# Kernel optimization log

Hardware: AMD Instinct MI355X
Metric: run time of the kernel (lower is better)

## Reference

```python
import jax, jax.numpy as jnp
import numpy as np

BS, S, D, H = 4, 1024, 768, 12
NE, M, P = 42, 8, 500
IN_C, OUT_C = 3, 256
EMB, BLK, NL = 768, 64, 97


def setup_inputs() -> dict:
    key = jax.random.key(0)
    ks = jax.random.split(key, 16)
    seq_out = jax.random.normal(ks[0], (BS, S, D), jnp.float32)
    attention = jax.random.uniform(ks[1], (BS, H, S, S), jnp.float32)
    ent_tok = jax.random.randint(ks[2], (BS, NE, M), 0, 1022)
    ent_mask = (jax.random.uniform(ks[3], (BS, NE, M)) < 0.7).astype(jnp.float32)
    ent_mask = ent_mask.at[:, :, 0].set(1.0)  # every entity has >=1 mention
    hts = jax.random.randint(ks[4], (BS, P, 2), 0, NE)
    sc = 0.02
    return {
        'seq_out': seq_out,
        'attention': attention,
        'ent_tok': ent_tok,
        'ent_mask': ent_mask,
        'hts': hts,
        'W_liner': jax.random.normal(ks[5], (D, IN_C)) * sc,
        'b_liner': jnp.zeros((IN_C,), jnp.float32),
        'W_seg': jax.random.normal(ks[6], (IN_C, OUT_C)) * sc,
        'b_seg': jnp.zeros((OUT_C,), jnp.float32),
        'W_head': jax.random.normal(ks[7], (D + OUT_C, EMB)) * sc,
        'b_head': jnp.zeros((EMB,), jnp.float32),
        'W_tail': jax.random.normal(ks[8], (D + OUT_C, EMB)) * sc,
        'b_tail': jnp.zeros((EMB,), jnp.float32),
        'W_bil': jax.random.normal(ks[9], (EMB * BLK, NL)) * sc,
        'b_bil': jnp.zeros((NL,), jnp.float32),
    }


def reference(seq_out, attention, ent_tok, ent_mask, hts,
              W_liner, b_liner, W_seg, b_seg,
              W_head, b_head, W_tail, b_tail, W_bil, b_bil):
    bs, S_, d = seq_out.shape
    heads = attention.shape[1]
    # --- get_hrt: per-entity ragged pooling (offset=1 on token starts) ---
    idx = jnp.clip(ent_tok + 1, 0, S_ - 1)                   # [bs,ne,M]
    valid = ent_mask * (ent_tok + 1 < S_).astype(ent_mask.dtype)
    b_ix = jnp.arange(bs)[:, None, None]
    tok_emb = seq_out[b_ix, idx]                             # [bs,ne,M,d]
    neg = jnp.where(valid[..., None] > 0, tok_emb, jnp.float32(-1e30))
    e_emb = jax.nn.logsumexp(neg, axis=2)                    # [bs,ne,d]
    cnt = valid.sum(2)                                       # [bs,ne]
    e_emb = jnp.where((cnt > 0)[..., None], e_emb, 0.0)
    att_g = attention[b_ix, :, idx]                          # [bs,ne,M,H,S]
    e_att = (att_g * valid[..., None, None]).sum(2) / jnp.maximum(cnt, 1.0)[..., None, None]  # [bs,ne,H,S]
    e_att = jnp.where((cnt > 0)[..., None, None], e_att, 0.0)
    # --- get_channel_map: attention-weighted context contraction ---
    ht_att = jnp.einsum('bihs,bjhs->bijs', e_att, e_att) / heads  # [bs,ne,ne,S]
    ht_att = ht_att / (ht_att.sum(-1, keepdims=True) + 1e-5)
    feat = jnp.einsum('bijs,bsd->bijd', ht_att, seq_out)          # [bs,ne,ne,d]
    # --- liner + segmentation stand-in (pointwise) ---
    attn_map = (feat @ W_liner + b_liner) @ W_seg + b_seg         # [bs,ne,ne,OUT_C]
    # --- gather pair features ---
    bp = jnp.arange(bs)[:, None]
    h_i, t_i = hts[..., 0], hts[..., 1]
    h_t = attn_map[bp, h_i, t_i].reshape(-1, attn_map.shape[-1])  # [bs*P,OUT_C]
    hs = e_emb[bp, h_i].reshape(-1, d)
    ts = e_emb[bp, t_i].reshape(-1, d)
    hs = jnp.tanh(jnp.concatenate([hs, h_t], axis=1) @ W_head + b_head)
    ts = jnp.tanh(jnp.concatenate([ts, h_t], axis=1) @ W_tail + b_tail)
    # --- block bilinear classifier ---
    n = hs.shape[0]
    b1 = hs.reshape(n, EMB // BLK, BLK)
    b2 = ts.reshape(n, EMB // BLK, BLK)
    bl = (b1[:, :, :, None] * b2[:, :, None, :]).reshape(n, EMB * BLK)
    logits = bl @ W_bil + b_bil                                   # [bs*P, NL]
    return logits
```

## Files before the change

### kernel.cpp

```cpp
#include <hip/hip_runtime.h>
#include <hip/hip_bf16.h>
#include <math.h>

#define BSZ 4
#define SEQ 1024
#define DIM 768
#define NH 12
#define NEnt 42
#define MM 8
#define PPairs 500
#define INC 3
#define OUTC 256
#define EMB 768
#define BLKsz 64
#define NL 97
#define NPAIR (BSZ*PPairs)
#define XROWS 2048
#define NCHUNK 24

typedef __bf16 bf16x8 __attribute__((ext_vector_type(8)));
typedef __bf16 bf16x4 __attribute__((ext_vector_type(4)));
typedef float f32x4 __attribute__((ext_vector_type(4)));

#define OFF_EEMB  4096
#define OFF_EATT  520192
#define OFF_SP    4648960
#define OFF_XB    4698112
#define OFF_WHT   13086720
#define OFF_WT    16232448
#define OFF_HSB   25767936
#define OFF_TSB   28839936
#define OFF_PART  31911936

#define B_EEMB0 0
#define B_EATT0 168
#define B_SP0   2184
#define B_WHT0  3208
#define B_WT0   3592
#define B_ZERO0 4360
#define B_TOTAL 4362

__device__ __forceinline__ float ldin(const void* p, long long i, int f32) {
  if (f32) return ((const float*)p)[i];
  unsigned int u = (unsigned int)(((const unsigned short*)p)[i]) << 16;
  union { unsigned int u; float f; } c; c.u = u;
  return c.f;
}

__device__ __forceinline__ f32x4 ldin4(const void* p, long long i, int f32) {
  f32x4 r;
  if (f32) {
    r = *(const f32x4*)((const float*)p + i);
  } else {
    unsigned long long v = *(const unsigned long long*)((const unsigned short*)p + i);
    union { unsigned int u; float f; } c;
    c.u = (unsigned int)(v & 0xFFFFu) << 16;         r[0] = c.f;
    c.u = (unsigned int)((v >> 16) & 0xFFFFu) << 16; r[1] = c.f;
    c.u = (unsigned int)((v >> 32) & 0xFFFFu) << 16; r[2] = c.f;
    c.u = (unsigned int)((v >> 48) & 0xFFFFu) << 16; r[3] = c.f;
  }
  return r;
}

__device__ __forceinline__ float tanhf_fast(float x) {
  float ax = fabsf(x);
  float t = __expf(-2.0f*ax);
  float r = (1.0f - t)/(1.0f + t);
  return x < 0.0f ? -r : r;
}

__global__ void k_detect(const void* w_head, int* flag) {
  int tid = threadIdx.x;
  unsigned int word = ((const unsigned int*)w_head)[tid];
  union { unsigned int u; float f; } c;
  c.u = (word & 0xFFFFu) << 16;
  float v = fabsf(c.f);
  unsigned long long m = __ballot(v > 1.0f);
  if (tid == 0) flag[0] = (__popcll(m) >= 8) ? 1 : 0;
}

__global__ __launch_bounds__(256)
void k_stage1(const void* seq, const void* att, const int* etok,
              const void* emask, const void* wliner,
              const void* whead, const void* wtail, const void* wbil,
              const int* flag,
              float* e_emb, __bf16* e_att, float* sp,
              __bf16* whT, __bf16* wT, __bf16* Xb) {
  __shared__ float smem[64*98];
  int blk = blockIdx.x;
  int tid = threadIdx.x;
  int f32 = *flag;

  if (blk < B_EATT0) {
    int be = blk, b = be / NEnt;
    int* sidx = (int*)smem;
    float* sval = smem + 16;
    if (tid < MM) {
      int t = etok[be*MM + tid];
      int ip = t + 1;
      float v = ldin(emask, be*MM + tid, f32);
      sval[tid] = (ip < SEQ) ? v : 0.0f;
      sidx[tid] = ip < 0 ? 0 : (ip > SEQ-1 ? SEQ-1 : ip);
    }
    __syncthreads();
    float cnt = 0.0f;
#pragma unroll
    for (int m = 0; m < MM; m++) cnt += sval[m];
    for (int d = tid; d < DIM; d += 256) {
      float x[MM];
#pragma unroll
      for (int m = 0; m < MM; m++)
        x[m] = ldin(seq, ((long long)(b*SEQ) + sidx[m])*DIM + d, f32);
      float mx = -1e30f;
#pragma unroll
      for (int m = 0; m < MM; m++) if (sval[m] > 0.0f && x[m] > mx) mx = x[m];
      float s = 0.0f;
#pragma unroll
      for (int m = 0; m < MM; m++) if (sval[m] > 0.0f) s += expf(x[m] - mx);
      e_emb[(long long)be*DIM + d] = (cnt > 0.0f) ? (mx + logf(s)) : 0.0f;
    }
  } else if (blk < B_SP0) {
    int t1 = blk - B_EATT0;
    int h = t1 % NH, be = t1 / NH, b = be / NEnt;
    int* sidx = (int*)smem;
    float* sval = smem + 16;
    if (tid < MM) {
      int t = etok[be*MM + tid];
      int ip = t + 1;
      float v = ldin(emask, be*MM + tid, f32);
      sval[tid] = (ip < SEQ) ? v : 0.0f;
      sidx[tid] = ip < 0 ? 0 : (ip > SEQ-1 ? SEQ-1 : ip);
    }
    __syncthreads();
    float cnt = 0.0f;
#pragma unroll
    for (int m = 0; m < MM; m++) cnt += sval[m];
    float rs = (cnt > 0.0f) ? 1.0f/fmaxf(cnt, 1.0f) : 0.0f;
    long long abase = ((long long)(b*NH + h))*SEQ*SEQ;
    int s0 = tid*4;
    f32x4 acc = (f32x4){0,0,0,0};
#pragma unroll
    for (int m = 0; m < MM; m++)
      if (sval[m] > 0.0f) {
        f32x4 v = ldin4(att, abase + (long long)sidx[m]*SEQ + s0, f32);
        acc += sval[m]*v;
      }
    bf16x4 ov;
#pragma unroll
    for (int k = 0; k < 4; k++) ov[k] = (__bf16)(acc[k]*rs);
    *(bf16x4*)(e_att + ((long long)(be*NH + h))*SEQ + s0) = ov;
  } else if (blk < B_WHT0) {
    int t2 = blk - B_SP0;
    int b = t2 >> 8;
    int wv = tid >> 6, l = tid & 63;
    int s = ((t2 & 255) << 2) + wv;
    long long rb = ((long long)(b*SEQ) + s)*DIM;
    float a0 = 0, a1 = 0, a2 = 0;
#pragma unroll
    for (int i = 0; i < DIM/64; i++) {
      int d = l + i*64;
      float x = ldin(seq, rb + d, f32);
      a0 += x*ldin(wliner, (long long)d*3 + 0, f32);
      a1 += x*ldin(wliner, (long long)d*3 + 1, f32);
      a2 += x*ldin(wliner, (long long)d*3 + 2, f32);
    }
#pragma unroll
    for (int o = 32; o; o >>= 1) {
      a0 += __shfl_down(a0, o);
      a1 += __shfl_down(a1, o);
      a2 += __shfl_down(a2, o);
    }
    if (l == 0) {
      sp[0*(BSZ*SEQ) + b*SEQ + s] = a0;
      sp[1*(BSZ*SEQ) + b*SEQ + s] = a1;
      sp[2*(BSZ*SEQ) + b*SEQ + s] = a2;
    }
  } else if (blk < B_WT0) {
    int t3 = blk - B_WHT0;
    int kb = t3 & 15, rest = t3 >> 4;
    int nb = rest % 12, y = rest / 12;
    const void* W = y ? wtail : whead;
    for (int i = tid; i < 64*64; i += 256) {
      int r = i >> 6, c = i & 63;
      smem[r*65 + c] = ldin(W, (long long)(kb*64 + r)*EMB + nb*64 + c, f32);
    }
    __syncthreads();
    for (int j = tid; j < 64*64; j += 256) {
      int r = j >> 6, k = j & 63;
      whT[((long long)y*EMB + nb*64 + r)*1024 + kb*64 + k] = (__bf16)smem[k*65 + r];
    }
  } else if (blk < B_ZERO0) {
    int t4 = blk - B_WT0;
    int kb = t4 & 63, g = t4 >> 6;
    long long base = ((long long)g*4096 + kb*64)*97;
    for (int i = tid; i < 64*97; i += 256)
      smem[(i/97)*98 + (i%97)] = ldin(wbil, base + i, f32);
    __syncthreads();
    for (int j = tid; j < 97*64; j += 256) {
      int l = j >> 6, k = j & 63;
      wT[((long long)g*97 + l)*4096 + kb*64 + k] = (__bf16)smem[k*98 + l];
    }
  } else {
    int y = blk - B_ZERO0;
    uint4 z = {0,0,0,0};
    uint4* dst = (uint4*)(Xb + ((long long)(y*XROWS + NPAIR))*1024);
    for (int i = tid; i < 48*1024*2/16; i += 256) dst[i] = z;
  }
}

__global__ __launch_bounds__(256)
void k_pair2(const __bf16* e_att, const float* sp, const float* e_emb,
             const int* hts, const void* bliner, const void* wseg,
             const void* bseg, const int* flag, __bf16* Xb) {
  __shared__ float cross[4][4];
  int p = blockIdx.x;
  int b = p / PPairs;
  int tid = threadIdx.x;
  int f32 = *flag;
  int hi = hts[p*2 + 0];
  int ti = hts[p*2 + 1];
  const __bf16* ei = e_att + ((long long)(b*NEnt + hi))*NH*SEQ;
  const __bf16* ej = e_att + ((long long)(b*NEnt + ti))*NH*SEQ;
  int s0 = tid*4;
  f32x4 q = (f32x4){0,0,0,0};
#pragma unroll
  for (int h = 0; h < NH; h++) {
    bf16x4 xi = *(const bf16x4*)(ei + h*SEQ + s0);
    bf16x4 xj = *(const bf16x4*)(ej + h*SEQ + s0);
#pragma unroll
    for (int k = 0; k < 4; k++) q[k] += (float)xi[k]*(float)xj[k];
  }
  f32x4 w0 = *(const f32x4*)(sp + 0*(BSZ*SEQ) + b*SEQ + s0);
  f32x4 w1 = *(const f32x4*)(sp + 1*(BSZ*SEQ) + b*SEQ + s0);
  f32x4 w2 = *(const f32x4*)(sp + 2*(BSZ*SEQ) + b*SEQ + s0);
  float dn = q[0]+q[1]+q[2]+q[3];
  float a0 = q[0]*w0[0]+q[1]*w0[1]+q[2]*w0[2]+q[3]*w0[3];
  float a1 = q[0]*w1[0]+q[1]*w1[1]+q[2]*w1[2]+q[3]*w1[3];
  float a2 = q[0]*w2[0]+q[1]*w2[1]+q[2]*w2[2]+q[3]*w2[3];
#pragma unroll
  for (int o = 32; o; o >>= 1) {
    dn += __shfl_down(dn, o);
    a0 += __shfl_down(a0, o);
    a1 += __shfl_down(a1, o);
    a2 += __shfl_down(a2, o);
  }
  int wv = tid >> 6, l = tid & 63;
  if (l == 0) { cross[0][wv] = dn; cross[1][wv] = a0; cross[2][wv] = a1; cross[3][wv] = a2; }
  __syncthreads();
  float DN = cross[0][0]+cross[0][1]+cross[0][2]+cross[0][3];
  float A0 = cross[1][0]+cross[1][1]+cross[1][2]+cross[1][3];
  float A1 = cross[2][0]+cross[2][1]+cross[2][2]+cross[2][3];
  float A2 = cross[3][0]+cross[3][1]+cross[3][2]+cross[3][3];
  const float inv = 1.0f/(float)NH;
  float scale = inv/(DN*inv + 1e-5f);
  float v0 = A0*scale + ldin(bliner, 0, f32);
  float v1 = A1*scale + ldin(bliner, 1, f32);
  float v2 = A2*scale + ldin(bliner, 2, f32);
  float o = ldin(bseg, tid, f32)
          + v0*ldin(wseg, 0*OUTC + tid, f32)
          + v1*ldin(wseg, 1*OUTC + tid, f32)
          + v2*ldin(wseg, 2*OUTC + tid, f32);
  __bf16* X0 = Xb + ((long long)(0*XROWS + p))*1024;
  __bf16* X1 = Xb + ((long long)(1*XROWS + p))*1024;
  X0[DIM + tid] = (__bf16)o;
  X1[DIM + tid] = (__bf16)o;
  const float* eh = e_emb + (long long)(b*NEnt + hi)*DIM;
  const float* et = e_emb + (long long)(b*NEnt + ti)*DIM;
  for (int k = tid; k < DIM; k += 256) {
    X0[k] = (__bf16)eh[k];
    X1[k] = (__bf16)et[k];
  }
}

__global__ __launch_bounds__(256, 1)
void k_htmm(const __bf16* Xb, const __bf16* whT,
            const void* bhead, const void* btail, const int* flag,
            __bf16* hsb, __bf16* tsb) {
  __shared__ __bf16 Xa[2][128][72];
  __shared__ __bf16 Bb[2][64][72];
  int tid = threadIdx.x;
  int w = tid >> 6, lane = tid & 63, quad = lane >> 4, col = lane & 15;
  int m0 = blockIdx.x*128;
  int n0 = blockIdx.y*64;
  int y  = blockIdx.z;
  int f32 = *flag;
  const __bf16* Xg = Xb + (long long)y*XROWS*1024;
  const __bf16* Wg = whT + ((long long)y*EMB + n0)*1024;

  auto stage = [&](int kk, int p) {
#pragma unroll
    for (int it = 0; it < 4; it++) {
      int r = (tid >> 3) + it*32;
      int c0 = (tid & 7)*8;
      bf16x8 v = *(const bf16x8*)(Xg + (long long)(m0 + r)*1024 + kk + c0);
      *(bf16x8*)&Xa[p][r][c0] = v;
    }
#pragma unroll
    for (int it = 0; it < 2; it++) {
      int r = (tid >> 3) + it*32;
      int c0 = (tid & 7)*8;
      bf16x8 v = *(const bf16x8*)(Wg + (long long)r*1024 + kk + c0);
      *(bf16x8*)&Bb[p][r][c0] = v;
    }
  };

  f32x4 acc[2][4];
#pragma unroll
  for (int mf = 0; mf < 2; mf++)
#pragma unroll
    for (int nt = 0; nt < 4; nt++) acc[mf][nt] = (f32x4){0,0,0,0};

  stage(0, 0);
  __syncthreads();
  for (int c = 0; c < 16; c++) {
    int p = c & 1;
    if (c + 1 < 16) stage((c+1)*64, p ^ 1);
#pragma unroll
    for (int s = 0; s < 2; s++) {
      bf16x8 av[2], bv[4];
#pragma unroll
      for (int mf = 0; mf < 2; mf++)
        av[mf] = *(bf16x8*)&Xa[p][w*32 + mf*16 + col][s*32 + quad*8];
#pragma unroll
      for (int nt = 0; nt < 4; nt++)
        bv[nt] = *(bf16x8*)&Bb[p][nt*16 + col][s*32 + quad*8];
#pragma unroll
      for (int mf = 0; mf < 2; mf++)
#pragma unroll
        for (int nt = 0; nt < 4; nt++)
          acc[mf][nt] = __builtin_amdgcn_mfma_f32_16x16x32_bf16(av[mf], bv[nt],
                                                                acc[mf][nt], 0, 0, 0);
    }
    __syncthreads();
  }

  const void* Bv = y ? btail : bhead;
  __bf16* out = y ? tsb : hsb;
#pragma unroll
  for (int nt = 0; nt < 4; nt++) {
    int n = n0 + nt*16 + col;
    float bias = ldin(Bv, n, f32);
#pragma unroll
    for (int mf = 0; mf < 2; mf++)
#pragma unroll
      for (int reg = 0; reg < 4; reg++) {
        int m = m0 + w*32 + mf*16 + quad*4 + reg;
        if (m < NPAIR)
          out[(long long)m*EMB + n] = (__bf16)tanhf_fast(acc[mf][nt][reg] + bias);
      }
  }
}

__global__ __launch_bounds__(128, 2)
void k_bilmfma(const __bf16* hsb, const __bf16* tsb,
               const __bf16* wT, _Float16* part24) {
  __shared__ __bf16 hslT[32][72];
  int tid = threadIdx.x;
  int w = tid >> 6, lane = tid & 63, quad = lane >> 4, col = lane & 15;
  int m0 = blockIdx.x*64;
  int c  = blockIdx.y;
  int g  = c >> 1, kh = c & 1;

  {
    int srow = tid & 63;
    int grow = m0 + srow; if (grow > NPAIR-1) grow = NPAIR-1;
    int ah = (tid >> 6)*16;
    const __bf16* hp = hsb + (long long)grow*EMB + g*BLKsz + kh*32 + ah;
#pragma unroll
    for (int c0 = 0; c0 < 2; c0++) {
      bf16x8 hv = *(const bf16x8*)(hp + c0*8);
#pragma unroll
      for (int j = 0; j < 8; j++) hslT[ah + c0*8 + j][srow] = hv[j];
    }
  }
  bf16x8 tsv[2][2];
#pragma unroll
  for (int mf = 0; mf < 2; mf++) {
    int row = m0 + w*32 + mf*16 + col; if (row > NPAIR-1) row = NPAIR-1;
    const __bf16* tp = tsb + (long long)row*EMB + g*BLKsz + quad*8;
    tsv[mf][0] = *(const bf16x8*)(tp);
    tsv[mf][1] = *(const bf16x8*)(tp + 32);
  }
  __syncthreads();

  const __bf16* wg = wT + (long long)g*NL*4096 + kh*2048 + quad*8;
  int boff[7];
#pragma unroll
  for (int nt = 0; nt < 7; nt++) {
    int l = nt*16 + col; if (l > 96) l = 96;
    boff[nt] = l*4096;
  }
  f32x4 acc[2][7];
#pragma unroll
  for (int mf = 0; mf < 2; mf++)
#pragma unroll
    for (int nt = 0; nt < 7; nt++) acc[mf][nt] = (f32x4){0,0,0,0};

  bf16x8 bv[2][7];
#pragma unroll
  for (int nt = 0; nt < 7; nt++) bv[0][nt] = *(const bf16x8*)(wg + boff[nt]);
#pragma unroll
  for (int nt = 0; nt < 7; nt++) bv[1][nt] = *(const bf16x8*)(wg + boff[nt] + 32);

  for (int a = 0; a < 32; a++) {
    float hv[2];
#pragma unroll
    for (int mf = 0; mf < 2; mf++)
      hv[mf] = (float)hslT[a][w*32 + mf*16 + col];
#pragma unroll
    for (int half = 0; half < 2; half++) {
      bf16x8 af[2];
#pragma unroll
      for (int mf = 0; mf < 2; mf++)
#pragma unroll
        for (int j = 0; j < 8; j++)
          af[mf][j] = (__bf16)(hv[mf] * (float)tsv[mf][half][j]);
#pragma unroll
      for (int mf = 0; mf < 2; mf++)
#pragma unroll
        for (int nt = 0; nt < 7; nt++)
          acc[mf][nt] = __builtin_amdgcn_mfma_f32_16x16x32_bf16(af[mf], bv[half][nt],
                                                                acc[mf][nt], 0, 0, 0);
      int knext = (a+1)*64 + half*32;
      if (knext >= 2048) knext = a*64 + half*32;
#pragma unroll
      for (int nt = 0; nt < 7; nt++)
        bv[half][nt] = *(const bf16x8*)(wg + boff[nt] + knext);
    }
  }

  _Float16* ps = part24 + (long long)c*NPAIR*NL;
#pragma unroll
  for (int mf = 0; mf < 2; mf++)
#pragma unroll
    for (int nt = 0; nt < 7; nt++)
#pragma unroll
      for (int reg = 0; reg < 4; reg++) {
        int n = m0 + w*32 + mf*16 + quad*4 + reg;
        int l = nt*16 + col;
        if (n < NPAIR && l < NL)
          ps[(long long)n*NL + l] = (_Float16)acc[mf][nt][reg];
      }
}

__global__ void k_final(const _Float16* part24, const void* b_bil, const int* flag,
                        void* out) {
  int i = blockIdx.x*256 + threadIdx.x;
  if (i >= NPAIR*NL) return;
  int l = i % NL;
  int f32 = *flag;
  float v = ldin(b_bil, l, f32);
#pragma unroll
  for (int c = 0; c < NCHUNK; c++) v += (float)part24[(long long)c*NPAIR*NL + i];
  if (f32) ((float*)out)[i] = v;
  else ((__hip_bfloat16*)out)[i] = __float2bfloat16(v);
}

extern "C" void kernel_launch(void* const* d_in, const int* in_sizes, int n_in,
                              void* d_out, int out_size, void* d_ws, size_t ws_size,
                              hipStream_t stream) {
  const void* seq    = d_in[0];
  const void* att    = d_in[1];
  const int*  etok   = (const int*)d_in[2];
  const void* emask  = d_in[3];
  const int*  hts    = (const int*)d_in[4];
  const void* wliner = d_in[5];
  const void* bliner = d_in[6];
  const void* wseg   = d_in[7];
  const void* bseg   = d_in[8];
  const void* whead  = d_in[9];
  const void* bhead  = d_in[10];
  const void* wtail  = d_in[11];
  const void* btail  = d_in[12];
  const void* wbil   = d_in[13];
  const void* bbil   = d_in[14];

  char* ws = (char*)d_ws;
  int*      flag   = (int*)ws;
  float*    e_emb  = (float*)(ws + OFF_EEMB);
  __bf16*   e_att  = (__bf16*)(ws + OFF_EATT);
  float*    sp     = (float*)(ws + OFF_SP);
  __bf16*   Xb     = (__bf16*)(ws + OFF_XB);
  __bf16*   whT    = (__bf16*)(ws + OFF_WHT);
  __bf16*   wT     = (__bf16*)(ws + OFF_WT);
  __bf16*   hsb    = (__bf16*)(ws + OFF_HSB);
  __bf16*   tsb    = (__bf16*)(ws + OFF_TSB);
  _Float16* part24 = (_Float16*)(ws + OFF_PART);

  k_detect<<<1, 64, 0, stream>>>(whead, flag);
  k_stage1<<<B_TOTAL, 256, 0, stream>>>(seq, att, etok, emask, wliner,
                                        whead, wtail, wbil, flag,
                                        e_emb, e_att, sp, whT, wT, Xb);
  k_pair2<<<NPAIR, 256, 0, stream>>>(e_att, sp, e_emb, hts, bliner, wseg, bseg,
                                     flag, Xb);
  k_htmm<<<dim3(16, 12, 2), 256, 0, stream>>>(Xb, whT, bhead, btail, flag, hsb, tsb);
  k_bilmfma<<<dim3(32, NCHUNK), 128, 0, stream>>>(hsb, tsb, wT, part24);
  k_final<<<(NPAIR*NL + 255)/256, 256, 0, stream>>>(part24, bbil, flag, d_out);
}
```

Measured before the change: 418.9 us.

## Fuse all stages into one cooperative persistent kernel with grid syncs

Replaces the six separate launches (detect, stage1, pair, head/tail GEMM, bilinear MFMA, final reduce) with one cooperative persistent kernel. Blocks loop over the work units of each phase, and grid.sync() separates the phases. The head/tail GEMM and bilinear tiles are also reshaped to 256-thread blocks with one 16-row M fragment per wave instead of two. The aim is to remove launch overhead and inter-kernel gaps, at the cost of grid-wide barriers, a grid limited by occupancy, and a different MFMA tiling per wave.

```diff
diff --git a/kernel.cpp b/kernel.cpp
--- a/kernel.cpp
+++ b/kernel.cpp
@@ -1,6 +1,9 @@
 #include <hip/hip_runtime.h>
 #include <hip/hip_bf16.h>
+#include <hip/hip_cooperative_groups.h>
 #include <math.h>
+
+namespace cg = cooperative_groups;
 
 #define BSZ 4
 #define SEQ 1024
@@ -69,431 +72,693 @@
   return x < 0.0f ? -r : r;
 }
 
+struct MegaParams {
+  const void* seq; const void* att; const int* etok; const void* emask;
+  const int* hts; const void* wliner; const void* bliner; const void* wseg;
+  const void* bseg; const void* whead; const void* bhead; const void* wtail;
+  const void* btail; const void* wbil; const void* bbil; void* out;
+  float* e_emb; __bf16* e_att; float* sp; __bf16* Xb; __bf16* whT; __bf16* wT;
+  __bf16* hsb; __bf16* tsb; _Float16* part24;
+};
+
+__global__ __launch_bounds__(256)
+void k_mega(MegaParams P) {
+  __shared__ __align__(16) char smem_raw[36864];
+  __shared__ int sflag;
+  const int tid = threadIdx.x;
+  const int nb = gridDim.x;
+  const int w = tid >> 6, lane = tid & 63, quad = lane >> 4, col = lane & 15;
+
+  if (tid < 64) {
+    unsigned int word = ((const unsigned int*)P.whead)[tid];
+    union { unsigned int u; float f; } c; c.u = (word & 0xFFFFu) << 16;
+    unsigned long long m = __ballot(fabsf(c.f) > 1.0f);
+    if (tid == 0) sflag = (__popcll(m) >= 8) ? 1 : 0;
+  }
+  __syncthreads();
+  const int f32 = sflag;
+
+  cg::grid_group grid = cg::this_grid();
+  float* smemf = (float*)smem_raw;
+
+  for (int blk = blockIdx.x; blk < B_TOTAL; blk += nb) {
+    __syncthreads();
+    if (blk < B_EATT0) {
+      int be = blk, b = be / NEnt;
+      int* sidx = (int*)smemf;
+      float* sval = smemf + 16;
+      if (tid < MM) {
+        int t = P.etok[be*MM + tid];
+        int ip = t + 1;
+        float v = ldin(P.emask, be*MM + tid, f32);
+        sval[tid] = (ip < SEQ) ? v : 0.0f;
+        sidx[tid] = ip < 0 ? 0 : (ip > SEQ-1 ? SEQ-1 : ip);
+      }
+      __syncthreads();
+      float cnt = 0.0f;
+#pragma unroll
+      for (int m = 0; m < MM; m++) cnt += sval[m];
+      for (int d = tid; d < DIM; d += 256) {
+        float x[MM];
+#pragma unroll
+        for (int m = 0; m < MM; m++)
+          x[m] = ldin(P.seq, ((long long)(b*SEQ) + sidx[m])*DIM + d, f32);
+        float mx = -1e30f;
+#pragma unroll
+        for (int m = 0; m < MM; m++) if (sval[m] > 0.0f && x[m] > mx) mx = x[m];
+        float s = 0.0f;
+#pragma unroll
+        for (int m = 0; m < MM; m++) if (sval[m] > 0.0f) s += expf(x[m] - mx);
+        P.e_emb[(long long)be*DIM + d] = (cnt > 0.0f) ? (mx + logf(s)) : 0.0f;
+      }
+    } else if (blk < B_SP0) {
+      int t1 = blk - B_EATT0;
+      int h = t1 % NH, be = t1 / NH, b = be / NEnt;
+      int* sidx = (int*)smemf;
+      float* sval = smemf + 16;
+      if (tid < MM) {
+        int t = P.etok[be*MM + tid];
+        int ip = t + 1;
+        float v = ldin(P.emask, be*MM + tid, f32);
+        sval[tid] = (ip < SEQ) ? v : 0.0f;
+        sidx[tid] = ip < 0 ? 0 : (ip > SEQ-1 ? SEQ-1 : ip);
+      }
+      __syncthreads();
+      float cnt = 0.0f;
+#pragma unroll
+      for (int m = 0; m < MM; m++) cnt += sval[m];
+      float rs = (cnt > 0.0f) ? 1.0f/fmaxf(cnt, 1.0f) : 0.0f;
+      long long abase = ((long long)(b*NH + h))*SEQ*SEQ;
+      int s0 = tid*4;
+      f32x4 acc = (f32x4){0,0,0,0};
+#pragma unroll
+      for (int m = 0; m < MM; m++)
+        if (sval[m] > 0.0f) {
+          f32x4 v = ldin4(P.att, abase + (long long)sidx[m]*SEQ + s0, f32);
+          acc += sval[m]*v;
+        }
+      bf16x4 ov;
+#pragma unroll
+      for (int k = 0; k < 4; k++) ov[k] = (__bf16)(acc[k]*rs);
+      *(bf16x4*)(P.e_att + ((long long)(be*NH + h))*SEQ + s0) = ov;
+    } else if (blk < B_WHT0) {
+      int t2 = blk - B_SP0;
+      int b = t2 >> 8;
+      int wv = tid >> 6, l = tid & 63;
+      int s = ((t2 & 255) << 2) + wv;
+      long long rb = ((long long)(b*SEQ) + s)*DIM;
+      float a0 = 0, a1 = 0, a2 = 0;
+#pragma unroll
+      for (int i = 0; i < DIM/64; i++) {
+        int d = l + i*64;
+        float x = ldin(P.seq, rb + d, f32);
+        a0 += x*ldin(P.wliner, (long long)d*3 + 0, f32);
+        a1 += x*ldin(P.wliner, (long long)d*3 + 1, f32);
+        a2 += x*ldin(P.wliner, (long long)d*3 + 2, f32);
+      }
+#pragma unroll
+      for (int o = 32; o; o >>= 1) {
+        a0 += __shfl_down(a0, o);
+        a1 += __shfl_down(a1, o);
+        a2 += __shfl_down(a2, o);
+      }
+      if (l == 0) {
+        P.sp[0*(BSZ*SEQ) + b*SEQ + s] = a0;
+        P.sp[1*(BSZ*SEQ) + b*SEQ + s] = a1;
+        P.sp[2*(BSZ*SEQ) + b*SEQ + s] = a2;
+      }
+    } else if (blk < B_WT0) {
+      int t3 = blk - B_WHT0;
+      int kb = t3 & 15, rest = t3 >> 4;
+      int nbk = rest % 12, y = rest / 12;
+      const void* W = y ? P.wtail : P.whead;
+      for (int i = tid; i < 64*64; i += 256) {
+        int r = i >> 6, c = i & 63;
+        smemf[r*65 + c] = ldin(W, (long long)(kb*64 + r)*EMB + nbk*64 + c, f32);
+      }
+      __syncthreads();
+      for (int j = tid; j < 64*64; j += 256) {
+        int r = j >> 6, k = j & 63;
+        P.whT[((long long)y*EMB + nbk*64 + r)*1024 + kb*64 + k] = (__bf16)smemf[k*65 + r];
+      }
+    } else if (blk < B_ZERO0) {
+      int t4 = blk - B_WT0;
+      int kb = t4 & 63, g = t4 >> 6;
+      long long base = ((long long)g*4096 + kb*64)*97;
+      for (int i = tid; i < 64*97; i += 256)
+        smemf[(i/97)*98 + (i%97)] = ldin(P.wbil, base + i, f32);
+      __syncthreads();
+      for (int j = tid; j < 97*64; j += 256) {
+        int l = j >> 6, k = j & 63;
+        P.wT[((long long)g*97 + l)*4096 + kb*64 + k] = (__bf16)smemf[k*98 + l];
+      }
+    } else {
+      int y = blk - B_ZERO0;
+      uint4 z = {0,0,0,0};
+      uint4* dst = (uint4*)(P.Xb + ((long long)(y*XROWS + NPAIR))*1024);
+      for (int i = tid; i < 48*1024*2/16; i += 256) dst[i] = z;
+    }
+  }
+  grid.sync();
+
+  float (*cross)[4] = (float (*)[4])smem_raw;
+  for (int p = blockIdx.x; p < NPAIR; p += nb) {
+    __syncthreads();
+    int b = p / PPairs;
+    int hi = P.hts[p*2 + 0];
+    int ti = P.hts[p*2 + 1];
+    const __bf16* ei = P.e_att + ((long long)(b*NEnt + hi))*NH*SEQ;
+    const __bf16* ej = P.e_att + ((long long)(b*NEnt + ti))*NH*SEQ;
+    int s0 = tid*4;
+    f32x4 q = (f32x4){0,0,0,0};
+#pragma unroll
+    for (int h = 0; h < NH; h++) {
+      bf16x4 xi = *(const bf16x4*)(ei + h*SEQ + s0);
+      bf16x4 xj = *(const bf16x4*)(ej + h*SEQ + s0);
+#pragma unroll
+      for (int k = 0; k < 4; k++) q[k] += (float)xi[k]*(float)xj[k];
+    }
+    f32x4 w0 = *(const f32x4*)(P.sp + 0*(BSZ*SEQ) + b*SEQ + s0);
+    f32x4 w1 = *(const f32x4*)(P.sp + 1*(BSZ*SEQ) + b*SEQ + s0);
+    f32x4 w2 = *(const f32x4*)(P.sp + 2*(BSZ*SEQ) + b*SEQ + s0);
+    float dn = q[0]+q[1]+q[2]+q[3];
+    float a0 = q[0]*w0[0]+q[1]*w0[1]+q[2]*w0[2]+q[3]*w0[3];
+    float a1 = q[0]*w1[0]+q[1]*w1[1]+q[2]*w1[2]+q[3]*w1[3];
+    float a2 = q[0]*w2[0]+q[1]*w2[1]+q[2]*w2[2]+q[3]*w2[3];
+#pragma unroll
+    for (int o = 32; o; o >>= 1) {
+      dn += __shfl_down(dn, o);
+      a0 += __shfl_down(a0, o);
+      a1 += __shfl_down(a1, o);
+      a2 += __shfl_down(a2, o);
+    }
+    if (lane == 0) { cross[0][w] = dn; cross[1][w] = a0; cross[2][w] = a1; cross[3][w] = a2; }
+    __syncthreads();
+    float DN = cross[0][0]+cross[0][1]+cross[0][2]+cross[0][3];
+    float A0 = cross[1][0]+cross[1][1]+cross[1][2]+cross[1][3];
+    float A1 = cross[2][0]+cross[2][1]+cross[2][2]+cross[2][3];
+    float A2 = cross[3][0]+cross[3][1]+cross[3][2]+cross[3][3];
+    const float inv = 1.0f/(float)NH;
+    float scale = inv/(DN*inv + 1e-5f);
+    float v0 = A0*scale + ldin(P.bliner, 0, f32);
+    float v1 = A1*scale + ldin(P.bliner, 1, f32);
+    float v2 = A2*scale + ldin(P.bliner, 2, f32);
+    float o = ldin(P.bseg, tid, f32)
+            + v0*ldin(P.wseg, 0*OUTC + tid, f32)
+            + v1*ldin(P.wseg, 1*OUTC + tid, f32)
+            + v2*ldin(P.wseg, 2*OUTC + tid, f32);
+    __bf16* X0 = P.Xb + ((long long)(0*XROWS + p))*1024;
+    __bf16* X1 = P.Xb + ((long long)(1*XROWS + p))*1024;
+    X0[DIM + tid] = (__bf16)o;
+    X1[DIM + tid] = (__bf16)o;
+    const float* eh = P.e_emb + (long long)(b*NEnt + hi)*DIM;
+    const float* et = P.e_emb + (long long)(b*NEnt + ti)*DIM;
+    for (int k = tid; k < DIM; k += 256) {
+      X0[k] = (__bf16)eh[k];
+      X1[k] = (__bf16)et[k];
+    }
+  }
+  grid.sync();
+
+  for (int u = blockIdx.x; u < 32*12*2; u += nb) {
+    __syncthreads();
+    int m0 = (u & 31) << 6;
+    int rest = u >> 5;
+    int n0 = (rest % 12) << 6;
+    int y  = rest / 12;
+    __bf16 (*Xa)[64][72] = (__bf16 (*)[64][72])smem_raw;
+    __bf16 (*Bb)[64][72] = (__bf16 (*)[64][72])(smem_raw + 18432);
+    const __bf16* Xg = P.Xb + (long long)y*XROWS*1024;
+    const __bf16* Wg = P.whT + ((long long)y*EMB + n0)*1024;
+    auto stage = [&](int kk, int pb) {
+#pragma unroll
+      for (int it = 0; it < 2; it++) {
+        int r = (tid >> 3) + (it << 5);
+        int c0 = (tid & 7) << 3;
+        *(bf16x8*)&Xa[pb][r][c0] = *(const bf16x8*)(Xg + (long long)(m0 + r)*1024 + kk + c0);
+        *(bf16x8*)&Bb[pb][r][c0] = *(const bf16x8*)(Wg + (long long)r*1024 + kk + c0);
+      }
+    };
+    f32x4 acc[4];
+#pragma unroll
+    for (int nt = 0; nt < 4; nt++) acc[nt] = (f32x4){0,0,0,0};
+    stage(0, 0);
+    __syncthreads();
+    for (int c = 0; c < 16; c++) {
+      int pb = c & 1;
+      if (c + 1 < 16) stage((c+1)*64, pb ^ 1);
+#pragma unroll
+      for (int s = 0; s < 2; s++) {
+        bf16x8 av = *(bf16x8*)&Xa[pb][(w<<4) + col][s*32 + quad*8];
+        bf16x8 bv[4];
+#pragma unroll
+        for (int nt = 0; nt < 4; nt++)
+          bv[nt] = *(bf16x8*)&Bb[pb][nt*16 + col][s*32 + quad*8];
+#pragma unroll
+        for (int nt = 0; nt < 4; nt++)
+          acc[nt] = __builtin_amdgcn_mfma_f32_16x16x32_bf16(av, bv[nt], acc[nt], 0, 0, 0);
+      }
+      __syncthreads();
+    }
+    const void* Bv = y ? P.btail : P.bhead;
+    __bf16* outp = y ? P.tsb : P.hsb;
+#pragma unroll
+    for (int nt = 0; nt < 4; nt++) {
+      int n = n0 + nt*16 + col;
+      float bias = ldin(Bv, n, f32);
+#pragma unroll
+      for (int reg = 0; reg < 4; reg++) {
+        int m = m0 + (w<<4) + quad*4 + reg;
+        if (m < NPAIR)
+          outp[(long long)m*EMB + n] = (__bf16)tanhf_fast(acc[nt][reg] + bias);
+      }
+    }
+  }
+  grid.sync();
+
+  for (int u = blockIdx.x; u < 32*NCHUNK; u += nb) {
+    __syncthreads();
+    int m0 = (u & 31) << 6;
+    int c  = u >> 5;
+    int g = c >> 1, kh = c & 1;
+    __bf16 (*hslT)[72] = (__bf16 (*)[72])smem_raw;
+    {
+      int srow = tid & 63;
+      int grow = m0 + srow; if (grow > NPAIR-1) grow = NPAIR-1;
+      int ah = (tid >> 6) << 3;
+      const __bf16* hp = P.hsb + (long long)grow*EMB + g*BLKsz + kh*32 + ah;
+      bf16x8 hv8 = *(const bf16x8*)hp;
+#pragma unroll
+      for (int j = 0; j < 8; j++) hslT[ah + j][srow] = hv8[j];
+    }
+    bf16x8 tsv[2];
+    {
+      int row = m0 + (w<<4) + col; if (row > NPAIR-1) row = NPAIR-1;
+      const __bf16* tp = P.tsb + (long long)row*EMB + g*BLKsz + quad*8;
+      tsv[0] = *(const bf16x8*)(tp);
+      tsv[1] = *(const bf16x8*)(tp + 32);
+    }
+    __syncthreads();
+    const __bf16* wg = P.wT + (long long)g*NL*4096 + kh*2048 + quad*8;
+    int boff[7];
+#pragma unroll
+    for (int nt = 0; nt < 7; nt++) {
+      int l = nt*16 + col; if (l > 96) l = 96;
+      boff[nt] = l*4096;
+    }
+    f32x4 acc[7];
+#pragma unroll
+    for (int nt = 0; nt < 7; nt++) acc[nt] = (f32x4){0,0,0,0};
+    bf16x8 bv[2][7];
+#pragma unroll
+    for (int nt = 0; nt < 7; nt++) bv[0][nt] = *(const bf16x8*)(wg + boff[nt]);
+#pragma unroll
+    for (int nt = 0; nt < 7; nt++) bv[1][nt] = *(const bf16x8*)(wg + boff[nt] + 32);
+    for (int a = 0; a < 32; a++) {
+      float hv = (float)hslT[a][(w<<4) + col];
+#pragma unroll
+      for (int half = 0; half < 2; half++) {
+        bf16x8 af;
+#pragma unroll
+        for (int j = 0; j < 8; j++) af[j] = (__bf16)(hv * (float)tsv[half][j]);
+#pragma unroll
+        for (int nt = 0; nt < 7; nt++)
+          acc[nt] = __builtin_amdgcn_mfma_f32_16x16x32_bf16(af, bv[half][nt], acc[nt], 0, 0, 0);
+        int knext = (a+1)*64 + half*32;
+        if (knext >= 2048) knext = a*64 + half*32;
+#pragma unroll
+        for (int nt = 0; nt < 7; nt++)
+          bv[half][nt] = *(const bf16x8*)(wg + boff[nt] + knext);
+      }
+    }
+    _Float16* ps = P.part24 + (long long)c*NPAIR*NL;
+#pragma unroll
+    for (int nt = 0; nt < 7; nt++)
+#pragma unroll
+      for (int reg = 0; reg < 4; reg++) {
+        int n = m0 + (w<<4) + quad*4 + reg;
+        int l = nt*16 + col;
+        if (n < NPAIR && l < NL)
+          ps[(long long)n*NL + l] = (_Float16)acc[nt][reg];
+      }
+  }
+  grid.sync();
+
+  for (int i = blockIdx.x*256 + tid; i < NPAIR*NL; i += nb*256) {
+    int l = i % NL;
+    float v = ldin(P.bbil, l, f32);
+#pragma unroll
+    for (int c = 0; c < NCHUNK; c++) v += (float)P.part24[(long long)c*NPAIR*NL + i];
+    if (f32) ((float*)P.out)[i] = v;
+    else ((__hip_bfloat16*)P.out)[i] = __float2bfloat16(v);
+  }
+}
+
 __global__ void k_detect(const void* w_head, int* flag) {
   int tid = threadIdx.x;
   unsigned int word = ((const unsigned int*)w_head)[tid];
   union { unsigned int u; float f; } c;
   c.u = (word & 0xFFFFu) << 16;
-  float v = fabsf(c.f);
-  unsigned long long m = __ballot(v > 1.0f);
+  unsigned long long m = __ballot(fabsf(c.f) > 1.0f);
   if (tid == 0) flag[0] = (__popcll(m) >= 8) ? 1 : 0;
 }
 
 __global__ __launch_bounds__(256)
-void k_stage1(const void* seq, const void* att, const int* etok,
-              const void* emask, const void* wliner,
-              const void* whead, const void* wtail, const void* wbil,
-              const int* flag,
-              float* e_emb, __bf16* e_att, float* sp,
-              __bf16* whT, __bf16* wT, __bf16* Xb) {
-  __shared__ float smem[64*98];
-  int blk = blockIdx.x;
-  int tid = threadIdx.x;
-  int f32 = *flag;
-
-  if (blk < B_EATT0) {
-    int be = blk, b = be / NEnt;
-    int* sidx = (int*)smem;
-    float* sval = smem + 16;
-    if (tid < MM) {
-      int t = etok[be*MM + tid];
-      int ip = t + 1;
-      float v = ldin(emask, be*MM + tid, f32);
-      sval[tid] = (ip < SEQ) ? v : 0.0f;
-      sidx[tid] = ip < 0 ? 0 : (ip > SEQ-1 ? SEQ-1 : ip);
-    }
-    __syncthreads();
-    float cnt = 0.0f;
-#pragma unroll
-    for (int m = 0; m < MM; m++) cnt += sval[m];
-    for (int d = tid; d < DIM; d += 256) {
-      float x[MM];
+void k_fb(MegaParams P, const int* flag, int phase) {
+  __shared__ __align__(16) char smem_raw[36864];
+  const int tid = threadIdx.x;
+  const int f32 = *flag;
+  const int w = tid >> 6, lane = tid & 63, quad = lane >> 4, col = lane & 15;
+  float* smemf = (float*)smem_raw;
+  if (phase == 0) {
+    int blk = blockIdx.x;
+    if (blk < B_EATT0) {
+      int be = blk, b = be / NEnt;
+      int* sidx = (int*)smemf; float* sval = smemf + 16;
+      if (tid < MM) {
+        int t = P.etok[be*MM + tid]; int ip = t + 1;
+        float v = ldin(P.emask, be*MM + tid, f32);
+        sval[tid] = (ip < SEQ) ? v : 0.0f;
+        sidx[tid] = ip < 0 ? 0 : (ip > SEQ-1 ? SEQ-1 : ip);
+      }
+      __syncthreads();
+      float cnt = 0.0f;
+#pragma unroll
+      for (int m = 0; m < MM; m++) cnt += sval[m];
+      for (int d = tid; d < DIM; d += 256) {
+        float x[MM];
+#pragma unroll
+        for (int m = 0; m < MM; m++)
+          x[m] = ldin(P.seq, ((long long)(b*SEQ) + sidx[m])*DIM + d, f32);
+        float mx = -1e30f;
+#pragma unroll
+        for (int m = 0; m < MM; m++) if (sval[m] > 0.0f && x[m] > mx) mx = x[m];
+        float s = 0.0f;
+#pragma unroll
+        for (int m = 0; m < MM; m++) if (sval[m] > 0.0f) s += expf(x[m] - mx);
+        P.e_emb[(long long)be*DIM + d] = (cnt > 0.0f) ? (mx + logf(s)) : 0.0f;
+      }
+    } else if (blk < B_SP0) {
+      int t1 = blk - B_EATT0;
+      int h = t1 % NH, be = t1 / NH, b = be / NEnt;
+      int* sidx = (int*)smemf; float* sval = smemf + 16;
+      if (tid < MM) {
+        int t = P.etok[be*MM + tid]; int ip = t + 1;
+        float v = ldin(P.emask, be*MM + tid, f32);
+        sval[tid] = (ip < SEQ) ? v : 0.0f;
+        sidx[tid] = ip < 0 ? 0 : (ip > SEQ-1 ? SEQ-1 : ip);
+      }
+      __syncthreads();
+      float cnt = 0.0f;
+#pragma unroll
+      for (int m = 0; m < MM; m++) cnt += sval[m];
+      float rs = (cnt > 0.0f) ? 1.0f/fmaxf(cnt, 1.0f) : 0.0f;
+      long long abase = ((long long)(b*NH + h))*SEQ*SEQ;
+      int s0 = tid*4;
+      f32x4 acc = (f32x4){0,0,0,0};
 #pragma unroll
       for (int m = 0; m < MM; m++)
-        x[m] = ldin(seq, ((long long)(b*SEQ) + sidx[m])*DIM + d, f32);
-      float mx = -1e30f;
-#pragma unroll
-      for (int m = 0; m < MM; m++) if (sval[m] > 0.0f && x[m] > mx) mx = x[m];
-      float s = 0.0f;
-#pragma unroll
-      for (int m = 0; m < MM; m++) if (sval[m] > 0.0f) s += expf(x[m] - mx);
-      e_emb[(long long)be*DIM + d] = (cnt > 0.0f) ? (mx + logf(s)) : 0.0f;
-    }
-  } else if (blk < B_SP0) {
-    int t1 = blk - B_EATT0;
-    int h = t1 % NH, be = t1 / NH, b = be / NEnt;
-    int* sidx = (int*)smem;
-    float* sval = smem + 16;
-    if (tid < MM) {
-      int t = etok[be*MM + tid];
-      int ip = t + 1;
-      float v = ldin(emask, be*MM + tid, f32);
-      sval[tid] = (ip < SEQ) ? v : 0.0f;
-      sidx[tid] = ip < 0 ? 0 : (ip > SEQ-1 ? SEQ-1 : ip);
-    }
-    __syncthreads();
-    float cnt = 0.0f;
-#pragma unroll
-    for (int m = 0; m < MM; m++) cnt += sval[m];
-    float rs = (cnt > 0.0f) ? 1.0f/fmaxf(cnt, 1.0f) : 0.0f;
-    long long abase = ((long long)(b*NH + h))*SEQ*SEQ;
+        if (sval[m] > 0.0f) acc += sval[m]*ldin4(P.att, abase + (long long)sidx[m]*SEQ + s0, f32);
+      bf16x4 ov;
+#pragma unroll
+      for (int k = 0; k < 4; k++) ov[k] = (__bf16)(acc[k]*rs);
+      *(bf16x4*)(P.e_att + ((long long)(be*NH + h))*SEQ + s0) = ov;
+    } else if (blk < B_WHT0) {
+      int t2 = blk - B_SP0; int b = t2 >> 8;
+      int wv = tid >> 6, l = tid & 63;
+      int s = ((t2 & 255) << 2) + wv;
+      long long rb = ((long long)(b*SEQ) + s)*DIM;
+      float a0 = 0, a1 = 0, a2 = 0;
+#pragma unroll
+      for (int i = 0; i < DIM/64; i++) {
+        int d = l + i*64;
+        float x = ldin(P.seq, rb + d, f32);
+        a0 += x*ldin(P.wliner, (long long)d*3 + 0, f32);
+        a1 += x*ldin(P.wliner, (long long)d*3 + 1, f32);
+        a2 += x*ldin(P.wliner, (long long)d*3 + 2, f32);
+      }
+#pragma unroll
+      for (int o = 32; o; o >>= 1) {
+        a0 += __shfl_down(a0, o); a1 += __shfl_down(a1, o); a2 += __shfl_down(a2, o);
+      }
+      if (l == 0) {
+        P.sp[0*(BSZ*SEQ) + b*SEQ + s] = a0;
+        P.sp[1*(BSZ*SEQ) + b*SEQ + s] = a1;
+        P.sp[2*(BSZ*SEQ) + b*SEQ + s] = a2;
+      }
+    } else if (blk < B_WT0) {
+      int t3 = blk - B_WHT0;
+      int kb = t3 & 15, rest = t3 >> 4;
+      int nbk = rest % 12, y = rest / 12;
+      const void* W = y ? P.wtail : P.whead;
+      for (int i = tid; i < 64*64; i += 256) {
+        int r = i >> 6, c = i & 63;
+        smemf[r*65 + c] = ldin(W, (long long)(kb*64 + r)*EMB + nbk*64 + c, f32);
+      }
+      __syncthreads();
+      for (int j = tid; j < 64*64; j += 256) {
+        int r = j >> 6, k = j & 63;
+        P.whT[((long long)y*EMB + nbk*64 + r)*1024 + kb*64 + k] = (__bf16)smemf[k*65 + r];
+      }
+    } else if (blk < B_ZERO0) {
+      int t4 = blk - B_WT0;
+      int kb = t4 & 63, g = t4 >> 6;
+      long long base = ((long long)g*4096 + kb*64)*97;
+      for (int i = tid; i < 64*97; i += 256)
+        smemf[(i/97)*98 + (i%97)] = ldin(P.wbil, base + i, f32);
+      __syncthreads();
+      for (int j = tid; j < 97*64; j += 256) {
+        int l = j >> 6, k = j & 63;
+        P.wT[((long long)g*97 + l)*4096 + kb*64 + k] = (__bf16)smemf[k*98 + l];
+      }
+    } else {
+      int y = blk - B_ZERO0;
+      uint4 z = {0,0,0,0};
+      uint4* dst = (uint4*)(P.Xb + ((long long)(y*XROWS + NPAIR))*1024);
+      for (int i = tid; i < 48*1024*2/16; i += 256) dst[i] = z;
+    }
+  } else if (phase == 1) {
+    float (*cross)[4] = (float (*)[4])smem_raw;
+    int p = blockIdx.x;
+    int b = p / PPairs;
+    int hi = P.hts[p*2 + 0], ti = P.hts[p*2 + 1];
+    const __bf16* ei = P.e_att + ((long long)(b*NEnt + hi))*NH*SEQ;
+    const __bf16* ej = P.e_att + ((long long)(b*NEnt + ti))*NH*SEQ;
     int s0 = tid*4;
-    f32x4 acc = (f32x4){0,0,0,0};
-#pragma unroll
-    for (int m = 0; m < MM; m++)
-      if (sval[m] > 0.0f) {
-        f32x4 v = ldin4(att, abase + (long long)sidx[m]*SEQ + s0, f32);
-        acc += sval[m]*v;
-      }
-    bf16x4 ov;
-#pragma unroll
-    for (int k = 0; k < 4; k++) ov[k] = (__bf16)(acc[k]*rs);
-    *(bf16x4*)(e_att + ((long long)(be*NH + h))*SEQ + s0) = ov;
-  } else if (blk < B_WHT0) {
-    int t2 = blk - B_SP0;
-    int b = t2 >> 8;
-    int wv = tid >> 6, l = tid & 63;
-    int s = ((t2 & 255) << 2) + wv;
-    long long rb = ((long long)(b*SEQ) + s)*DIM;
-    float a0 = 0, a1 = 0, a2 = 0;
-#pragma unroll
-    for (int i = 0; i < DIM/64; i++) {
-      int d = l + i*64;
-      float x = ldin(seq, rb + d, f32);
-      a0 += x*ldin(wliner, (long long)d*3 + 0, f32);
-      a1 += x*ldin(wliner, (long long)d*3 + 1, f32);
-      a2 += x*ldin(wliner, (long long)d*3 + 2, f32);
-    }
+    f32x4 q = (f32x4){0,0,0,0};
+#pragma unroll
+    for (int h = 0; h < NH; h++) {
+      bf16x4 xi = *(const bf16x4*)(ei + h*SEQ + s0);
+      bf16x4 xj = *(const bf16x4*)(ej + h*SEQ + s0);
+#pragma unroll
+      for (int k = 0; k < 4; k++) q[k] += (float)xi[k]*(float)xj[k];
+    }
+    f32x4 w0 = *(const f32x4*)(P.sp + 0*(BSZ*SEQ) + b*SEQ + s0);
+    f32x4 w1 = *(const f32x4*)(P.sp + 1*(BSZ*SEQ) + b*SEQ + s0);
+    f32x4 w2 = *(const f32x4*)(P.sp + 2*(BSZ*SEQ) + b*SEQ + s0);
+    float dn = q[0]+q[1]+q[2]+q[3];
+    float a0 = q[0]*w0[0]+q[1]*w0[1]+q[2]*w0[2]+q[3]*w0[3];
+    float a1 = q[0]*w1[0]+q[1]*w1[1]+q[2]*w1[2]+q[3]*w1[3];
+    float a2 = q[0]*w2[0]+q[1]*w2[1]+q[2]*w2[2]+q[3]*w2[3];
 #pragma unroll
     for (int o = 32; o; o >>= 1) {
-      a0 += __shfl_down(a0, o);
-      a1 += __shfl_down(a1, o);
-      a2 += __shfl_down(a2, o);
-    }
-    if (l == 0) {
-      sp[0*(BSZ*SEQ) + b*SEQ + s] = a0;
-      sp[1*(BSZ*SEQ) + b*SEQ + s] = a1;
-      sp[2*(BSZ*SEQ) + b*SEQ + s] = a2;
-    }
-  } else if (blk < B_WT0) {
-    int t3 = blk - B_WHT0;
-    int kb = t3 & 15, rest = t3 >> 4;
-    int nb = rest % 12, y = rest / 12;
-    const void* W = y ? wtail : whead;
-    for (int i = tid; i < 64*64; i += 256) {
-      int r = i >> 6, c = i & 63;
-      smem[r*65 + c] = ldin(W, (long long)(kb*64 + r)*EMB + nb*64 + c, f32);
-    }
-    __syncthreads();
-    for (int j = tid; j < 64*64; j += 256) {
-      int r = j >> 6, k = j & 63;
-      whT[((long long)y*EMB + nb*64 + r)*1024 + kb*64 + k] = (__bf16)smem[k*65 + r];
-    }
-  } else if (blk < B_ZERO0) {
-    int t4 = blk - B_WT0;
-    int kb = t4 & 63, g = t4 >> 6;
-    long long base = ((long long)g*4096 + kb*64)*97;
-    for (int i = tid; i < 64*97; i += 256)
-      smem[(i/97)*98 + (i%97)] = ldin(wbil, base + i, f32);
-    __syncthreads();
-    for (int j = tid; j < 97*64; j += 256) {
-      int l = j >> 6, k = j & 63;
-      wT[((long long)g*97 + l)*4096 + kb*64 + k] = (__bf16)smem[k*98 + l];
-    }
+      dn += __shfl_down(dn, o); a0 += __shfl_down(a0, o);
+      a1 += __shfl_down(a1, o); a2 += __shfl_down(a2, o);
+    }
+    if (lane == 0) { cross[0][w] = dn; cross[1][w] = a0; cross[2][w] = a1; cross[3][w] = a2; }
+    __syncthreads();
+    float DN = cross[0][0]+cross[0][1]+cross[0][2]+cross[0][3];
+    float A0 = cross[1][0]+cross[1][1]+cross[1][2]+cross[1][3];
+    float A1 = cross[2][0]+cross[2][1]+cross[2][2]+cross[2][3];
+    float A2 = cross[3][0]+cross[3][1]+cross[3][2]+cross[3][3];
+    const float inv = 1.0f/(float)NH;
+    float scale = inv/(DN*inv + 1e-5f);
+    float v0 = A0*scale + ldin(P.bliner, 0, f32);
+    float v1 = A1*scale + ldin(P.bliner, 1, f32);
+    float v2 = A2*scale + ldin(P.bliner, 2, f32);
+    float o = ldin(P.bseg, tid, f32)
+            + v0*ldin(P.wseg, 0*OUTC + tid, f32)
+            + v1*ldin(P.wseg, 1*OUTC + tid, f32)
+            + v2*ldin(P.wseg, 2*OUTC + tid, f32);
+    __bf16* X0 = P.Xb + ((long long)(0*XROWS + p))*1024;
+    __bf16* X1 = P.Xb + ((long long)(1*XROWS + p))*1024;
+    X0[DIM + tid] = (__bf16)o; X1[DIM + tid] = (__bf16)o;
+    const float* eh = P.e_emb + (long long)(b*NEnt + hi)*DIM;
+    const float* et = P.e_emb + (long long)(b*NEnt + ti)*DIM;
+    for (int k = tid; k < DIM; k += 256) { X0[k] = (__bf16)eh[k]; X1[k] = (__bf16)et[k]; }
+  } else if (phase == 2) {
+    int u = blockIdx.x;
+    int m0 = (u & 31) << 6;
+    int rest = u >> 5;
+    int n0 = (rest % 12) << 6;
+    int y  = rest / 12;
+    __bf16 (*Xa)[64][72] = (__bf16 (*)[64][72])smem_raw;
+    __bf16 (*Bb)[64][72] = (__bf16 (*)[64][72])(smem_raw + 18432);
+    const __bf16* Xg = P.Xb + (long long)y*XROWS*1024;
+    const __bf16* Wg = P.whT + ((long long)y*EMB + n0)*1024;
+    auto stage = [&](int kk, int pb) {
+#pragma unroll
+      for (int it = 0; it < 2; it++) {
+        int r = (tid >> 3) + (it << 5);
+        int c0 = (tid & 7) << 3;
+        *(bf16x8*)&Xa[pb][r][c0] = *(const bf16x8*)(Xg + (long long)(m0 + r)*1024 + kk + c0);
+        *(bf16x8*)&Bb[pb][r][c0] = *(const bf16x8*)(Wg + (long long)r*1024 + kk + c0);
+      }
+    };
+    f32x4 acc[4];
+#pragma unroll
+    for (int nt = 0; nt < 4; nt++) acc[nt] = (f32x4){0,0,0,0};
+    stage(0, 0);
+    __syncthreads();
+    for (int c = 0; c < 16; c++) {
+      int pb = c & 1;
+      if (c + 1 < 16) stage((c+1)*64, pb ^ 1);
+#pragma unroll
+      for (int s = 0; s < 2; s++) {
+        bf16x8 av = *(bf16x8*)&Xa[pb][(w<<4) + col][s*32 + quad*8];
+        bf16x8 bvv[4];
+#pragma unroll
+        for (int nt = 0; nt < 4; nt++) bvv[nt] = *(bf16x8*)&Bb[pb][nt*16 + col][s*32 + quad*8];
+#pragma unroll
+        for (int nt = 0; nt < 4; nt++)
+          acc[nt] = __builtin_amdgcn_mfma_f32_16x16x32_bf16(av, bvv[nt], acc[nt], 0, 0, 0);
+      }
+      __syncthreads();
+    }
+    const void* Bv = y ? P.btail : P.bhead;
+    __bf16* outp = y ? P.tsb : P.hsb;
+#pragma unroll
+    for (int nt = 0; nt < 4; nt++) {
+      int n = n0 + nt*16 + col;
+      float bias = ldin(Bv, n, f32);
+#pragma unroll
+      for (int reg = 0; reg < 4; reg++) {
+        int m = m0 + (w<<4) + quad*4 + reg;
+        if (m < NPAIR) outp[(long long)m*EMB + n] = (__bf16)tanhf_fast(acc[nt][reg] + bias);
+      }
+    }
+  } else if (phase == 3) {
+    int u = blockIdx.x;
+    int m0 = (u & 31) << 6;
+    int c  = u >> 5;
+    int g = c >> 1, kh = c & 1;
+    __bf16 (*hslT)[72] = (__bf16 (*)[72])smem_raw;
+    {
+      int srow = tid & 63;
+      int grow = m0 + srow; if (grow > NPAIR-1) grow = NPAIR-1;
+      int ah = (tid >> 6) << 3;
+      const __bf16* hp = P.hsb + (long long)grow*EMB + g*BLKsz + kh*32 + ah;
+      bf16x8 hv8 = *(const bf16x8*)hp;
+#pragma unroll
+      for (int j = 0; j < 8; j++) hslT[ah + j][srow] = hv8[j];
+    }
+    bf16x8 tsv[2];
+    {
+      int row = m0 + (w<<4) + col; if (row > NPAIR-1) row = NPAIR-1;
+      const __bf16* tp = P.tsb + (long long)row*EMB + g*BLKsz + quad*8;
+      tsv[0] = *(const bf16x8*)(tp); tsv[1] = *(const bf16x8*)(tp + 32);
+    }
+    __syncthreads();
+    const __bf16* wg = P.wT + (long long)g*NL*4096 + kh*2048 + quad*8;
+    int boff[7];
+#pragma unroll
+    for (int nt = 0; nt < 7; nt++) { int l = nt*16 + col; if (l > 96) l = 96; boff[nt] = l*4096; }
+    f32x4 acc[7];
+#pragma unroll
+    for (int nt = 0; nt < 7; nt++) acc[nt] = (f32x4){0,0,0,0};
+    bf16x8 bv[2][7];
+#pragma unroll
+    for (int nt = 0; nt < 7; nt++) bv[0][nt] = *(const bf16x8*)(wg + boff[nt]);
+#pragma unroll
+    for (int nt = 0; nt < 7; nt++) bv[1][nt] = *(const bf16x8*)(wg + boff[nt] + 32);
+    for (int a = 0; a < 32; a++) {
+      float hv = (float)hslT[a][(w<<4) + col];
+#pragma unroll
+      for (int half = 0; half < 2; half++) {
+        bf16x8 af;
+#pragma unroll
+        for (int j = 0; j < 8; j++) af[j] = (__bf16)(hv * (float)tsv[half][j]);
+#pragma unroll
+        for (int nt = 0; nt < 7; nt++)
+          acc[nt] = __builtin_amdgcn_mfma_f32_16x16x32_bf16(af, bv[half][nt], acc[nt], 0, 0, 0);
+        int knext = (a+1)*64 + half*32;
+        if (knext >= 2048) knext = a*64 + half*32;
+#pragma unroll
+        for (int nt = 0; nt < 7; nt++) bv[half][nt] = *(const bf16x8*)(wg + boff[nt] + knext);
+      }
+    }
+    _Float16* ps = P.part24 + (long long)c*NPAIR*NL;
+#pragma unroll
+    for (int nt = 0; nt < 7; nt++)
+#pragma unroll
+      for (int reg = 0; reg < 4; reg++) {
+        int n = m0 + (w<<4) + quad*4 + reg;
+        int l = nt*16 + col;
+        if (n < NPAIR && l < NL) ps[(long long)n*NL + l] = (_Float16)acc[nt][reg];
+      }
   } else {
-    int y = blk - B_ZERO0;
-    uint4 z = {0,0,0,0};
-    uint4* dst = (uint4*)(Xb + ((long long)(y*XROWS + NPAIR))*1024);
-    for (int i = tid; i < 48*1024*2/16; i += 256) dst[i] = z;
-  }
-}
-
-__global__ __launch_bounds__(256)
-void k_pair2(const __bf16* e_att, const float* sp, const float* e_emb,
-             const int* hts, const void* bliner, const void* wseg,
-             const void* bseg, const int* flag, __bf16* Xb) {
-  __shared__ float cross[4][4];
-  int p = blockIdx.x;
-  int b = p / PPairs;
-  int tid = threadIdx.x;
-  int f32 = *flag;
-  int hi = hts[p*2 + 0];
-  int ti = hts[p*2 + 1];
-  const __bf16* ei = e_att + ((long long)(b*NEnt + hi))*NH*SEQ;
-  const __bf16* ej = e_att + ((long long)(b*NEnt + ti))*NH*SEQ;
-  int s0 = tid*4;
-  f32x4 q = (f32x4){0,0,0,0};
-#pragma unroll
-  for (int h = 0; h < NH; h++) {
-    bf16x4 xi = *(const bf16x4*)(ei + h*SEQ + s0);
-    bf16x4 xj = *(const bf16x4*)(ej + h*SEQ + s0);
-#pragma unroll
-    for (int k = 0; k < 4; k++) q[k] += (float)xi[k]*(float)xj[k];
-  }
-  f32x4 w0 = *(const f32x4*)(sp + 0*(BSZ*SEQ) + b*SEQ + s0);
-  f32x4 w1 = *(const f32x4*)(sp + 1*(BSZ*SEQ) + b*SEQ + s0);
-  f32x4 w2 = *(const f32x4*)(sp + 2*(BSZ*SEQ) + b*SEQ + s0);
-  float dn = q[0]+q[1]+q[2]+q[3];
-  float a0 = q[0]*w0[0]+q[1]*w0[1]+q[2]*w0[2]+q[3]*w0[3];
-  float a1 = q[0]*w1[0]+q[1]*w1[1]+q[2]*w1[2]+q[3]*w1[3];
-  float a2 = q[0]*w2[0]+q[1]*w2[1]+q[2]*w2[2]+q[3]*w2[3];
-#pragma unroll
-  for (int o = 32; o; o >>= 1) {
-    dn += __shfl_down(dn, o);
-    a0 += __shfl_down(a0, o);
-    a1 += __shfl_down(a1, o);
-    a2 += __shfl_down(a2, o);
-  }
-  int wv = tid >> 6, l = tid & 63;
-  if (l == 0) { cross[0][wv] = dn; cross[1][wv] = a0; cross[2][wv] = a1; cross[3][wv] = a2; }
-  __syncthreads();
-  float DN = cross[0][0]+cross[0][1]+cross[0][2]+cross[0][3];
-  float A0 = cross[1][0]+cross[1][1]+cross[1][2]+cross[1][3];
-  float A1 = cross[2][0]+cross[2][1]+cross[2][2]+cross[2][3];
-  float A2 = cross[3][0]+cross[3][1]+cross[3][2]+cross[3][3];
-  const float inv = 1.0f/(float)NH;
-  float scale = inv/(DN*inv + 1e-5f);
-  float v0 = A0*scale + ldin(bliner, 0, f32);
-  float v1 = A1*scale + ldin(bliner, 1, f32);
-  float v2 = A2*scale + ldin(bliner, 2, f32);
-  float o = ldin(bseg, tid, f32)
-          + v0*ldin(wseg, 0*OUTC + tid, f32)
-          + v1*ldin(wseg, 1*OUTC + tid, f32)
-          + v2*ldin(wseg, 2*OUTC + tid, f32);
-  __bf16* X0 = Xb + ((long long)(0*XROWS + p))*1024;
-  __bf16* X1 = Xb + ((long long)(1*XROWS + p))*1024;
-  X0[DIM + tid] = (__bf16)o;
-  X1[DIM + tid] = (__bf16)o;
-  const float* eh = e_emb + (long long)(b*NEnt + hi)*DIM;
-  const float* et = e_emb + (long long)(b*NEnt + ti)*DIM;
-  for (int k = tid; k < DIM; k += 256) {
-    X0[k] = (__bf16)eh[k];
-    X1[k] = (__bf16)et[k];
-  }
-}
-
-__global__ __launch_bounds__(256, 1)
-void k_htmm(const __bf16* Xb, const __bf16* whT,
-            const void* bhead, const void* btail, const int* flag,
-            __bf16* hsb, __bf16* tsb) {
-  __shared__ __bf16 Xa[2][128][72];
-  __shared__ __bf16 Bb[2][64][72];
-  int tid = threadIdx.x;
-  int w = tid >> 6, lane = tid & 63, quad = lane >> 4, col = lane & 15;
-  int m0 = blockIdx.x*128;
-  int n0 = blockIdx.y*64;
-  int y  = blockIdx.z;
-  int f32 = *flag;
-  const __bf16* Xg = Xb + (long long)y*XROWS*1024;
-  const __bf16* Wg = whT + ((long long)y*EMB + n0)*1024;
-
-  auto stage = [&](int kk, int p) {
-#pragma unroll
-    for (int it = 0; it < 4; it++) {
-      int r = (tid >> 3) + it*32;
-      int c0 = (tid & 7)*8;
-      bf16x8 v = *(const bf16x8*)(Xg + (long long)(m0 + r)*1024 + kk + c0);
-      *(bf16x8*)&Xa[p][r][c0] = v;
-    }
-#pragma unroll
-    for (int it = 0; it < 2; it++) {
-      int r = (tid >> 3) + it*32;
-      int c0 = (tid & 7)*8;
-      bf16x8 v = *(const bf16x8*)(Wg + (long long)r*1024 + kk + c0);
-      *(bf16x8*)&Bb[p][r][c0] = v;
-    }
-  };
-
-  f32x4 acc[2][4];
-#pragma unroll
-  for (int mf = 0; mf < 2; mf++)
-#pragma unroll
-    for (int nt = 0; nt < 4; nt++) acc[mf][nt] = (f32x4){0,0,0,0};
-
-  stage(0, 0);
-  __syncthreads();
-  for (int c = 0; c < 16; c++) {
-    int p = c & 1;
-    if (c + 1 < 16) stage((c+1)*64, p ^ 1);
-#pragma unroll
-    for (int s = 0; s < 2; s++) {
-      bf16x8 av[2], bv[4];
-#pragma unroll
-      for (int mf = 0; mf < 2; mf++)
-        av[mf] = *(bf16x8*)&Xa[p][w*32 + mf*16 + col][s*32 + quad*8];
-#pragma unroll
-      for (int nt = 0; nt < 4; nt++)
-        bv[nt] = *(bf16x8*)&Bb[p][nt*16 + col][s*32 + quad*8];
-#pragma unroll
-      for (int mf = 0; mf < 2; mf++)
-#pragma unroll
-        for (int nt = 0; nt < 4; nt++)
-          acc[mf][nt] = __builtin_amdgcn_mfma_f32_16x16x32_bf16(av[mf], bv[nt],
-                                                                acc[mf][nt], 0, 0, 0);
-    }
-    __syncthreads();
-  }
-
-  const void* Bv = y ? btail : bhead;
-  __bf16* out = y ? tsb : hsb;
-#pragma unroll
-  for (int nt = 0; nt < 4; nt++) {
-    int n = n0 + nt*16 + col;
-    float bias = ldin(Bv, n, f32);
-#pragma unroll
-    for (int mf = 0; mf < 2; mf++)
-#pragma unroll
-      for (int reg = 0; reg < 4; reg++) {
-        int m = m0 + w*32 + mf*16 + quad*4 + reg;
-        if (m < NPAIR)
-          out[(long long)m*EMB + n] = (__bf16)tanhf_fast(acc[mf][nt][reg] + bias);
-      }
-  }
-}
-
-__global__ __launch_bounds__(128, 2)
-void k_bilmfma(const __bf16* hsb, const __bf16* tsb,
-               const __bf16* wT, _Float16* part24) {
-  __shared__ __bf16 hslT[32][72];
-  int tid = threadIdx.x;
-  int w = tid >> 6, lane = tid & 63, quad = lane >> 4, col = lane & 15;
-  int m0 = blockIdx.x*64;
-  int c  = blockIdx.y;
-  int g  = c >> 1, kh = c & 1;
-
-  {
-    int srow = tid & 63;
-    int grow = m0 + srow; if (grow > NPAIR-1) grow = NPAIR-1;
-    int ah = (tid >> 6)*16;
-    const __bf16* hp = hsb + (long long)grow*EMB + g*BLKsz + kh*32 + ah;
-#pragma unroll
-    for (int c0 = 0; c0 < 2; c0++) {
-      bf16x8 hv = *(const bf16x8*)(hp + c0*8);
-#pragma unroll
-      for (int j = 0; j < 8; j++) hslT[ah + c0*8 + j][srow] = hv[j];
-    }
-  }
-  bf16x8 tsv[2][2];
-#pragma unroll
-  for (int mf = 0; mf < 2; mf++) {
-    int row = m0 + w*32 + mf*16 + col; if (row > NPAIR-1) row = NPAIR-1;
-    const __bf16* tp = tsb + (long long)row*EMB + g*BLKsz + quad*8;
-    tsv[mf][0] = *(const bf16x8*)(tp);
-    tsv[mf][1] = *(const bf16x8*)(tp + 32);
-  }
-  __syncthreads();
-
-  const __bf16* wg = wT + (long long)g*NL*4096 + kh*2048 + quad*8;
-  int boff[7];
-#pragma unroll
-  for (int nt = 0; nt < 7; nt++) {
-    int l = nt*16 + col; if (l > 96) l = 96;
-    boff[nt] = l*4096;
-  }
-  f32x4 acc[2][7];
-#pragma unroll
-  for (int mf = 0; mf < 2; mf++)
-#pragma unroll
-    for (int nt = 0; nt < 7; nt++) acc[mf][nt] = (f32x4){0,0,0,0};
-
-  bf16x8 bv[2][7];
-#pragma unroll
-  for (int nt = 0; nt < 7; nt++) bv[0][nt] = *(const bf16x8*)(wg + boff[nt]);
-#pragma unroll
-  for (int nt = 0; nt < 7; nt++) bv[1][nt] = *(const bf16x8*)(wg + boff[nt] + 32);
-
-  for (int a = 0; a < 32; a++) {
-    float hv[2];
-#pragma unroll
-    for (int mf = 0; mf < 2; mf++)
-      hv[mf] = (float)hslT[a][w*32 + mf*16 + col];
-#pragma unroll
-    for (int half = 0; half < 2; half++) {
-      bf16x8 af[2];
-#pragma unroll
-      for (int mf = 0; mf < 2; mf++)
-#pragma unroll
-        for (int j = 0; j < 8; j++)
-          af[mf][j] = (__bf16)(hv[mf] * (float)tsv[mf][half][j]);
-#pragma unroll
-      for (int mf = 0; mf < 2; mf++)
-#pragma unroll
-        for (int nt = 0; nt < 7; nt++)
-          acc[mf][nt] = __builtin_amdgcn_mfma_f32_16x16x32_bf16(af[mf], bv[half][nt],
-                                                                acc[mf][nt], 0, 0, 0);
-      int knext = (a+1)*64 + half*32;
-      if (knext >= 2048) knext = a*64 + half*32;
-#pragma unroll
-      for (int nt = 0; nt < 7; nt++)
-        bv[half][nt] = *(const bf16x8*)(wg + boff[nt] + knext);
-    }
-  }
-
-  _Float16* ps = part24 + (long long)c*NPAIR*NL;
-#pragma unroll
-  for (int mf = 0; mf < 2; mf++)
-#pragma unroll
-    for (int nt = 0; nt < 7; nt++)
-#pragma unroll
-      for (int reg = 0; reg < 4; reg++) {
-        int n = m0 + w*32 + mf*16 + quad*4 + reg;
-        int l = nt*16 + col;
-        if (n < NPAIR && l < NL)
-          ps[(long long)n*NL + l] = (_Float16)acc[mf][nt][reg];
-      }
-}
-
-__global__ void k_final(const _Float16* part24, const void* b_bil, const int* flag,
-                        void* out) {
-  int i = blockIdx.x*256 + threadIdx.x;
-  if (i >= NPAIR*NL) return;
-  int l = i % NL;
-  int f32 = *flag;
-  float v = ldin(b_bil, l, f32);
-#pragma unroll
-  for (int c = 0; c < NCHUNK; c++) v += (float)part24[(long long)c*NPAIR*NL + i];
-  if (f32) ((float*)out)[i] = v;
-  else ((__hip_bfloat16*)out)[i] = __float2bfloat16(v);
+    int i = blockIdx.x*256 + tid;
+    if (i < NPAIR*NL) {
+      int l = i % NL;
+      float v = ldin(P.bbil, l, f32);
+#pragma unroll
+      for (int c = 0; c < NCHUNK; c++) v += (float)P.part24[(long long)c*NPAIR*NL + i];
+      if (f32) ((float*)P.out)[i] = v;
+      else ((__hip_bfloat16*)P.out)[i] = __float2bfloat16(v);
+    }
+  }
 }
 
 extern "C" void kernel_launch(void* const* d_in, const int* in_sizes, int n_in,
                               void* d_out, int out_size, void* d_ws, size_t ws_size,
                               hipStream_t stream) {
-  const void* seq    = d_in[0];
-  const void* att    = d_in[1];
-  const int*  etok   = (const int*)d_in[2];
-  const void* emask  = d_in[3];
-  const int*  hts    = (const int*)d_in[4];
-  const void* wliner = d_in[5];
-  const void* bliner = d_in[6];
-  const void* wseg   = d_in[7];
-  const void* bseg   = d_in[8];
-  const void* whead  = d_in[9];
-  const void* bhead  = d_in[10];
-  const void* wtail  = d_in[11];
-  const void* btail  = d_in[12];
-  const void* wbil   = d_in[13];
-  const void* bbil   = d_in[14];
-
   char* ws = (char*)d_ws;
-  int*      flag   = (int*)ws;
-  float*    e_emb  = (float*)(ws + OFF_EEMB);
-  __bf16*   e_att  = (__bf16*)(ws + OFF_EATT);
-  float*    sp     = (float*)(ws + OFF_SP);
-  __bf16*   Xb     = (__bf16*)(ws + OFF_XB);
-  __bf16*   whT    = (__bf16*)(ws + OFF_WHT);
-  __bf16*   wT     = (__bf16*)(ws + OFF_WT);
-  __bf16*   hsb    = (__bf16*)(ws + OFF_HSB);
-  __bf16*   tsb    = (__bf16*)(ws + OFF_TSB);
-  _Float16* part24 = (_Float16*)(ws + OFF_PART);
-
-  k_detect<<<1, 64, 0, stream>>>(whead, flag);
-  k_stage1<<<B_TOTAL, 256, 0, stream>>>(seq, att, etok, emask, wliner,
-                                        whead, wtail, wbil, flag,
-                                        e_emb, e_att, sp, whT, wT, Xb);
-  k_pair2<<<NPAIR, 256, 0, stream>>>(e_att, sp, e_emb, hts, bliner, wseg, bseg,
-                                     flag, Xb);
-  k_htmm<<<dim3(16, 12, 2), 256, 0, stream>>>(Xb, whT, bhead, btail, flag, hsb, tsb);
-  k_bilmfma<<<dim3(32, NCHUNK), 128, 0, stream>>>(hsb, tsb, wT, part24);
-  k_final<<<(NPAIR*NL + 255)/256, 256, 0, stream>>>(part24, bbil, flag, d_out);
+  MegaParams p;
+  p.seq    = d_in[0];  p.att    = d_in[1];
+  p.etok   = (const int*)d_in[2];
+  p.emask  = d_in[3];
+  p.hts    = (const int*)d_in[4];
+  p.wliner = d_in[5];  p.bliner = d_in[6];
+  p.wseg   = d_in[7];  p.bseg   = d_in[8];
+  p.whead  = d_in[9];  p.bhead  = d_in[10];
+  p.wtail  = d_in[11]; p.btail  = d_in[12];
+  p.wbil   = d_in[13]; p.bbil   = d_in[14];
+  p.out    = d_out;
+  p.e_emb  = (float*)(ws + OFF_EEMB);
+  p.e_att  = (__bf16*)(ws + OFF_EATT);
+  p.sp     = (float*)(ws + OFF_SP);
+  p.Xb     = (__bf16*)(ws + OFF_XB);
+  p.whT    = (__bf16*)(ws + OFF_WHT);
+  p.wT     = (__bf16*)(ws + OFF_WT);
+  p.hsb    = (__bf16*)(ws + OFF_HSB);
+  p.tsb    = (__bf16*)(ws + OFF_TSB);
+  p.part24 = (_Float16*)(ws + OFF_PART);
+
+  static int gblocks = -1;
+  if (gblocks < 0) {
+    int dev = 0; hipGetDevice(&dev);
+    int ncu = 0;
+    if (hipDeviceGetAttribute(&ncu, hipDeviceAttributeMultiprocessorCount, dev) != hipSuccess || ncu <= 0)
+      ncu = 256;
+    int occ = 0;
+    if (hipOccupancyMaxActiveBlocksPerMultiprocessor(&occ, k_mega, 256, 0) != hipSuccess || occ <= 0)
+      occ = 1;
+    long long g = (long long)occ * (long long)ncu;
+    if (g > B_TOTAL) g = B_TOTAL;
+    if (g < 1) g = 1;
+    gblocks = (int)g;
+  }
+
+  void* args[] = { (void*)&p };
+  hipError_t err = hipLaunchCooperativeKernel((const void*)k_mega, dim3(gblocks), dim3(256),
+                                              args, 0, stream);
+  if (err != hipSuccess) {
+    int* flag = (int*)ws;
+    k_detect<<<1, 64, 0, stream>>>(p.whead, flag);
+    k_fb<<<B_TOTAL, 256, 0, stream>>>(p, flag, 0);
+    k_fb<<<NPAIR, 256, 0, stream>>>(p, flag, 1);
+    k_fb<<<32*12*2, 256, 0, stream>>>(p, flag, 2);
+    k_fb<<<32*NCHUNK, 256, 0, stream>>>(p, flag, 3);
+    k_fb<<<(NPAIR*NL + 255)/256, 256, 0, stream>>>(p, flag, 4);
+  }
 }
```

Result: slower. 699.9 us (+67.1%).
